# Kernel tuning notes

Hardware: AMD Instinct MI355X
Metric: run time of the kernel (lower is better)

Reference implementation:

```python
import jax, jax.numpy as jnp
import numpy as np

NUM_GROUPS = 32
EPS = 1e-6


def group_norm(x, gamma, beta):
    # x: [B, C, H, W]
    B, C, H, W = x.shape
    xg = x.reshape(B, NUM_GROUPS, C // NUM_GROUPS, H, W)
    mu = jnp.mean(xg, axis=(2, 3, 4), keepdims=True)
    var = jnp.var(xg, axis=(2, 3, 4), keepdims=True)
    xg = (xg - mu) * jax.lax.rsqrt(var + EPS)
    x = xg.reshape(B, C, H, W)
    return x * gamma[None, :, None, None] + beta[None, :, None, None]


def conv1x1(x, w, b):
    # x: [B, C, H, W], w: [O, C], b: [O]
    return jnp.einsum('bchw,oc->bohw', x, w) + b[None, :, None, None]


def setup_inputs() -> dict:
    key = jax.random.key(0)
    C = 512
    B, H, W = 4, 64, 64
    ks = jax.random.split(key, 10)
    s = 1.0 / np.sqrt(C)
    inp = {
        'x': jax.random.normal(ks[0], (B, C, H, W), dtype=jnp.float32),
        'gamma': jnp.ones((C,), dtype=jnp.float32),
        'beta': jnp.zeros((C,), dtype=jnp.float32),
        'wq': jax.random.normal(ks[1], (C, C), dtype=jnp.float32) * s,
        'bq': jnp.zeros((C,), dtype=jnp.float32),
        'wk': jax.random.normal(ks[2], (C, C), dtype=jnp.float32) * s,
        'bk': jnp.zeros((C,), dtype=jnp.float32),
        'wv': jax.random.normal(ks[3], (C, C), dtype=jnp.float32) * s,
        'bv': jnp.zeros((C,), dtype=jnp.float32),
        'wo': jax.random.normal(ks[4], (C, C), dtype=jnp.float32) * s,
        'bo': jnp.zeros((C,), dtype=jnp.float32),
    }
    return inp


def reference(x, gamma, beta, wq, bq, wk, bk, wv, bv, wo, bo):
    B, C, H, W = x.shape
    h = group_norm(x, gamma, beta)
    q = conv1x1(h, wq, bq).reshape(B, C, H * W)  # [B, C, S]
    k = conv1x1(h, wk, bk).reshape(B, C, H * W)
    v = conv1x1(h, wv, bv).reshape(B, C, H * W)
    scale = C ** (-0.5)
    # scores[b, S, s] = sum_c q[b, c, S] * k[b, c, s]
    w = jnp.einsum('bcS,bcs->bSs', q, k) * scale
    w = jax.nn.softmax(w, axis=-1)
    # out[b, c, S] = sum_s w[b, S, s] * v[b, c, s]
    hattn = jnp.einsum('bSs,bcs->bcS', w, v).reshape(B, C, H, W)
    out = conv1x1(hattn, wo, bo)
    return x + out
```

## Files before the change

kernel.cpp:

```cpp
#include <hip/hip_runtime.h>

#define B_   4
#define C_   512
#define S_   4096
#define G_   32
#define CPG_ 16
#define EPS_ 1e-6f

typedef unsigned short u16;
typedef __bf16 bf16x8 __attribute__((ext_vector_type(8)));
typedef float  f32x4  __attribute__((ext_vector_type(4)));

__device__ __forceinline__ u16 f2bf(float f) {
  unsigned u = __float_as_uint(f);
  u += 0x7fffu + ((u >> 16) & 1u);
  return (u16)(u >> 16);
}
__device__ __forceinline__ float bf2f(u16 h) {
  return __uint_as_float((unsigned)h << 16);
}

__device__ __forceinline__ void g2lds16(const void* g, void* l) {
  __builtin_amdgcn_global_load_lds(
      (const __attribute__((address_space(1))) void*)g,
      (__attribute__((address_space(3))) void*)l, 16, 0, 0);
}

#define BAR()    __builtin_amdgcn_s_barrier()
#define SCHED0() __builtin_amdgcn_sched_barrier(0)
#define WAITV4   asm volatile("s_waitcnt vmcnt(4)" ::: "memory")
#define WAITV3   asm volatile("s_waitcnt vmcnt(3)" ::: "memory")
#define WAITV0   asm volatile("s_waitcnt vmcnt(0)" ::: "memory")

__device__ __forceinline__ void xcd_swz(int& bx, int& by, int& bz) {
  const int gx = gridDim.x, gy = gridDim.y;
  const int nwg = gx * gy * (int)gridDim.z;
  const int flat = blockIdx.x + gx * (blockIdx.y + gy * blockIdx.z);
  const int q = nwg >> 3;
  const int nf = (flat & 7) * q + (flat >> 3);
  bx = nf % gx;
  const int r = nf / gx;
  by = r % gy;
  bz = r / gy;
}

__global__ __launch_bounds__(256) void f32_to_bf16(const float* __restrict__ in,
                                                   u16* __restrict__ out, int n) {
  int i = blockIdx.x * 256 + threadIdx.x;
  if (i < n) out[i] = f2bf(in[i]);
}

__global__ __launch_bounds__(256) void concat_bias(const float* __restrict__ a,
                                                   const float* __restrict__ b,
                                                   float* __restrict__ o) {
  int i = blockIdx.x * 256 + threadIdx.x;
  o[i] = (i < 512) ? a[i] : b[i - 512];
}

__global__ __launch_bounds__(256) void gn_stats(const float* __restrict__ x,
                                                float* __restrict__ stats) {
  const int bg = blockIdx.x;
  const float4* p4 = (const float4*)(x + (size_t)bg * (CPG_ * S_));
  float s = 0.f, ss = 0.f;
  const int tid = threadIdx.x;
  for (int i = tid; i < CPG_ * S_ / 4; i += 256) {
    float4 v = p4[i];
    s  += v.x + v.y + v.z + v.w;
    ss += v.x * v.x + v.y * v.y + v.z * v.z + v.w * v.w;
  }
#pragma unroll
  for (int o = 32; o; o >>= 1) { s += __shfl_xor(s, o, 64); ss += __shfl_xor(ss, o, 64); }
  __shared__ float sm[8];
  const int wid = tid >> 6, lane = tid & 63;
  if (lane == 0) { sm[wid * 2] = s; sm[wid * 2 + 1] = ss; }
  __syncthreads();
  if (tid == 0) {
    s  = sm[0] + sm[2] + sm[4] + sm[6];
    ss = sm[1] + sm[3] + sm[5] + sm[7];
    const float inv = 1.f / (float)(CPG_ * S_);
    float mu = s * inv;
    float var = ss * inv - mu * mu;
    stats[bg * 2]     = mu;
    stats[bg * 2 + 1] = rsqrtf(var + EPS_);
  }
}

__global__ __launch_bounds__(256) void gn_apply_t(const float* __restrict__ x,
                                                  const float* __restrict__ gamma,
                                                  const float* __restrict__ beta,
                                                  const float* __restrict__ stats,
                                                  u16* __restrict__ ht) {
  __shared__ float tile[32][33];
  const int b = blockIdx.z, c0 = blockIdx.y * 32, s0 = blockIdx.x * 32;
  const int tx = threadIdx.x, ty = threadIdx.y;
#pragma unroll
  for (int i = 0; i < 4; ++i) {
    const int c  = c0 + ty + i * 8;
    const float mu = stats[(b * G_ + (c >> 4)) * 2];
    const float rs = stats[(b * G_ + (c >> 4)) * 2 + 1];
    const float v  = x[((size_t)b * C_ + c) * S_ + s0 + tx];
    tile[ty + i * 8][tx] = (v - mu) * rs * gamma[c] + beta[c];
  }
  __syncthreads();
#pragma unroll
  for (int i = 0; i < 4; ++i) {
    const int s = s0 + ty + i * 8;
    ht[((size_t)b * S_ + s) * C_ + c0 + tx] = f2bf(tile[tx][ty + i * 8]);
  }
}

#define STAGE_A(T, KS) do {                                                  \
    const int _sl = (2 * (T) + (KS)) & 3;                                    \
    const size_t _ko = (size_t)(T) * 64 + (KS) * 32;                         \
    g2lds16(Asrc + _ko,  &As[_sl][wid * 512]);                               \
    g2lds16(Asrc2 + _ko, &As[_sl][4096 + wid * 512]);                        \
  } while (0)
#define STAGE_B(T, KS) do {                                                  \
    const int _sl = (2 * (T) + (KS)) & 3;                                    \
    const size_t _ko = (size_t)(T) * 64 + (KS) * 32;                         \
    g2lds16(Bsrc + _ko,  &Bs[_sl][wid * 512]);                               \
    g2lds16(Bsrc2 + _ko, &Bs[_sl][4096 + wid * 512]);                        \
  } while (0)
#define LDB4(SL)                                                             \
  _Pragma("unroll") for (int i = 0; i < 4; ++i)                              \
      bfr[i] = *(const bf16x8*)&Bs[(SL)][bbase + i * 512];
#define LDA4(SL, MH)                                                         \
  _Pragma("unroll") for (int i = 0; i < 4; ++i)                              \
      af[i] = *(const bf16x8*)&As[(SL)][abase + ((MH) * 4 + i) * 512];
#define MFMA16(MH) do {                                                      \
    __builtin_amdgcn_s_setprio(1);                                           \
    _Pragma("unroll") for (int mi = 0; mi < 4; ++mi)                         \
    _Pragma("unroll") for (int ni = 0; ni < 4; ++ni)                         \
      acc[(MH) * 4 + mi][ni] = __builtin_amdgcn_mfma_f32_16x16x32_bf16(      \
          af[mi], bfr[ni], acc[(MH) * 4 + mi][ni], 0, 0, 0);                 \
    __builtin_amdgcn_s_setprio(0);                                           \
  } while (0)

template <int BIAS_MODE>
__global__ __launch_bounds__(512, 2) void gemm256(
    const u16* __restrict__ Ag, int lda, long sA,
    const u16* __restrict__ Bg, int ldb, long sB,
    u16* __restrict__ Cg, int ldc, long sC,
    const float* __restrict__ bias, float alpha, int K) {
  __shared__ u16 As[4][8192];
  __shared__ u16 Bs[4][8192];
  int bx, by, bz;
  xcd_swz(bx, by, bz);
  const u16* A  = Ag + (size_t)bz * sA;
  const u16* Bm = Bg + (size_t)bz * sB;
  u16* Cb = Cg + (size_t)bz * sC;
  const int bm = by * 256, bn = bx * 256;
  const int tid = threadIdx.x;
  const int wid = tid >> 6, lane = tid & 63;
  const int wm = (wid >> 2) * 128, wn = (wid & 3) * 64;
  const int lr = lane & 15, lh = lane >> 4;

  const int srow = wid * 16 + (lane >> 2);
  const int sg   = (lane & 3) ^ ((srow >> 1) & 3);
  const u16* Asrc  = A  + (size_t)(bm + srow) * lda + sg * 8;
  const u16* Asrc2 = Asrc + (size_t)128 * lda;
  const u16* Bsrc  = Bm + (size_t)(bn + srow) * ldb + sg * 8;
  const u16* Bsrc2 = Bsrc + (size_t)128 * ldb;

  const int swz   = (lh ^ ((lr >> 1) & 3)) << 3;
  const int abase = (wm + lr) * 32 + swz;
  const int bbase = (wn + lr) * 32 + swz;

  float bias_v[4] = {0.f, 0.f, 0.f, 0.f};
  if (BIAS_MODE == 1) {
#pragma unroll
    for (int nf = 0; nf < 4; ++nf) bias_v[nf] = bias[bn + wn + nf * 16 + lr];
  }
  SCHED0();

  f32x4 acc[8][4];
  const f32x4 zero = {0.f, 0.f, 0.f, 0.f};
#pragma unroll
  for (int i = 0; i < 8; ++i)
#pragma unroll
    for (int j = 0; j < 4; ++j) acc[i][j] = zero;

  STAGE_A(0, 0); STAGE_B(0, 0); STAGE_A(0, 1); STAGE_B(0, 1);

  const int nt = K >> 6;
  for (int t = 0; t < nt; ++t) {
    const int s0 = (2 * t) & 3, s1 = s0 + 1;
    const bool pre = (t + 1 < nt);
    bf16x8 bfr[4], af[4];
    WAITV4;
    BAR(); SCHED0();
    LDB4(s0);
    LDA4(s0, 0);
    if (pre) STAGE_A(t + 1, 0);
    MFMA16(0);
    BAR(); SCHED0();
    LDA4(s0, 1);
    if (pre) STAGE_B(t + 1, 0);
    MFMA16(1);
    if (pre) { WAITV4; } else { WAITV0; }
    BAR(); SCHED0();
    LDB4(s1);
    LDA4(s1, 0);
    if (pre) STAGE_A(t + 1, 1);
    MFMA16(0);
    BAR(); SCHED0();
    LDA4(s1, 1);
    if (pre) STAGE_B(t + 1, 1);
    MFMA16(1);
  }
  SCHED0();

#pragma unroll
  for (int mf = 0; mf < 8; ++mf) {
    const int row0 = bm + wm + mf * 16 + lh * 4;
#pragma unroll
    for (int nf = 0; nf < 4; ++nf) {
      const int col = bn + wn + nf * 16 + lr;
#pragma unroll
      for (int r = 0; r < 4; ++r)
        Cb[(size_t)(row0 + r) * ldc + col] = f2bf(acc[mf][nf][r] * alpha + bias_v[nf]);
    }
  }
}

__global__ __launch_bounds__(512, 2) void gemm256pv(
    const u16* __restrict__ Ag, int lda, long sA,
    const u16* __restrict__ Bg, int ldb, long sB,
    u16* __restrict__ Cg, int ldc, long sC, int K) {
  __shared__ u16 As[4][8192];
  __shared__ u16 Bs[4][4096];
  int bx, by, bz;
  xcd_swz(bx, by, bz);
  const u16* A  = Ag + (size_t)bz * sA;
  const u16* Bm = Bg + (size_t)bz * sB;
  u16* Cb = Cg + (size_t)bz * sC;
  const int bm = by * 256, bn = bx * 128;
  const int tid = threadIdx.x;
  const int wid = tid >> 6, lane = tid & 63;
  const int wm = (wid >> 1) * 64, wn = (wid & 1) * 64;
  const int lr = lane & 15, lh = lane >> 4;

  const int srow = wid * 16 + (lane >> 2);
  const int sg   = (lane & 3) ^ ((srow >> 1) & 3);
  const u16* Asrc  = A  + (size_t)(bm + srow) * lda + sg * 8;
  const u16* Asrc2 = Asrc + (size_t)128 * lda;
  const u16* Bsrc  = Bm + (size_t)(bn + srow) * ldb + sg * 8;

  const int swz   = (lh ^ ((lr >> 1) & 3)) << 3;
  const int abase = (wm + lr) * 32 + swz;
  const int bbase = (wn + lr) * 32 + swz;

#define PSTAGE_A(T, KS) do {                                                 \
    const int _sl = (2 * (T) + (KS)) & 3;                                    \
    const size_t _ko = (size_t)(T) * 64 + (KS) * 32;                         \
    g2lds16(Asrc + _ko,  &As[_sl][wid * 512]);                               \
    g2lds16(Asrc2 + _ko, &As[_sl][4096 + wid * 512]);                        \
  } while (0)
#define PSTAGE_B(T, KS) do {                                                 \
    const int _sl = (2 * (T) + (KS)) & 3;                                    \
    const size_t _ko = (size_t)(T) * 64 + (KS) * 32;                         \
    g2lds16(Bsrc + _ko, &Bs[_sl][wid * 512]);                                \
  } while (0)

  f32x4 acc[4][4];
  const f32x4 zero = {0.f, 0.f, 0.f, 0.f};
#pragma unroll
  for (int i = 0; i < 4; ++i)
#pragma unroll
    for (int j = 0; j < 4; ++j) acc[i][j] = zero;

  PSTAGE_A(0, 0); PSTAGE_B(0, 0); PSTAGE_A(0, 1); PSTAGE_B(0, 1);

  const int nt = K >> 6;
  for (int t = 0; t < nt; ++t) {
    const int s0 = (2 * t) & 3, s1 = s0 + 1;
    const bool pre = (t + 1 < nt);
    bf16x8 bfr[4], af[4];
    WAITV3;
    BAR(); SCHED0();
    _Pragma("unroll") for (int i = 0; i < 4; ++i)
        bfr[i] = *(const bf16x8*)&Bs[s0][bbase + i * 512];
    _Pragma("unroll") for (int i = 0; i < 4; ++i)
        af[i] = *(const bf16x8*)&As[s0][abase + i * 512];
    if (pre) { PSTAGE_A(t + 1, 0); PSTAGE_B(t + 1, 0); }
    __builtin_amdgcn_s_setprio(1);
#pragma unroll
    for (int mi = 0; mi < 4; ++mi)
#pragma unroll
      for (int ni = 0; ni < 4; ++ni)
        acc[mi][ni] = __builtin_amdgcn_mfma_f32_16x16x32_bf16(af[mi], bfr[ni], acc[mi][ni], 0, 0, 0);
    __builtin_amdgcn_s_setprio(0);
    if (pre) { WAITV3; } else { WAITV0; }
    BAR(); SCHED0();
    _Pragma("unroll") for (int i = 0; i < 4; ++i)
        bfr[i] = *(const bf16x8*)&Bs[s1][bbase + i * 512];
    _Pragma("unroll") for (int i = 0; i < 4; ++i)
        af[i] = *(const bf16x8*)&As[s1][abase + i * 512];
    if (pre) { PSTAGE_A(t + 1, 1); PSTAGE_B(t + 1, 1); }
    __builtin_amdgcn_s_setprio(1);
#pragma unroll
    for (int mi = 0; mi < 4; ++mi)
#pragma unroll
      for (int ni = 0; ni < 4; ++ni)
        acc[mi][ni] = __builtin_amdgcn_mfma_f32_16x16x32_bf16(af[mi], bfr[ni], acc[mi][ni], 0, 0, 0);
    __builtin_amdgcn_s_setprio(0);
  }
  SCHED0();

#pragma unroll
  for (int mf = 0; mf < 4; ++mf) {
    const int row0 = bm + wm + mf * 16 + lh * 4;
#pragma unroll
    for (int nf = 0; nf < 4; ++nf) {
      const int col = bn + wn + nf * 16 + lr;
#pragma unroll
      for (int r = 0; r < 4; ++r)
        Cb[(size_t)(row0 + r) * ldc + col] = f2bf(acc[mf][nf][r]);
    }
  }
}

#define GBM 128
#define GBN 128
#define GBK 64

template <int BIAS_MODE, int OUT_MODE>
__global__ __launch_bounds__(256) void gemm_abT(
    const u16* __restrict__ Ag, int lda, long sA,
    const u16* __restrict__ Bg, int ldb, long sB,
    void* __restrict__ Cg, int ldc, long sC,
    const float* __restrict__ bias, float alpha,
    const float* __restrict__ xres, int K) {
  __shared__ u16 As[GBM * GBK];
  __shared__ u16 Bs[GBN * GBK];
  const int bz = blockIdx.z;
  const u16* A    = Ag + (size_t)bz * sA;
  const u16* Bmat = Bg + (size_t)bz * sB;
  const int bm = blockIdx.y * GBM, bn = blockIdx.x * GBN;
  const int tid = threadIdx.x;
  const int wid = tid >> 6, lane = tid & 63;
  const int wm = (wid >> 1) * 64, wn = (wid & 1) * 64;
  const int lr = lane & 15, lh = lane >> 4;
  const int srow = lane >> 3, scol = (lane & 7) * 8;

  f32x4 acc[4][4];
  const f32x4 zero = {0.f, 0.f, 0.f, 0.f};
#pragma unroll
  for (int i = 0; i < 4; ++i)
#pragma unroll
    for (int j = 0; j < 4; ++j) acc[i][j] = zero;

  for (int k0 = 0; k0 < K; k0 += GBK) {
    __syncthreads();
#pragma unroll
    for (int i = 0; i < 4; ++i) {
      const int chunk = wid * 4 + i;
      const int row   = chunk * 8 + srow;
      g2lds16(A    + (size_t)(bm + row) * lda + (k0 + scol), &As[chunk * 512]);
      g2lds16(Bmat + (size_t)(bn + row) * ldb + (k0 + scol), &Bs[chunk * 512]);
    }
    __syncthreads();
#pragma unroll
    for (int ks = 0; ks < 2; ++ks) {
      bf16x8 a_[4], b_[4];
#pragma unroll
      for (int m = 0; m < 4; ++m)
        a_[m] = *(const bf16x8*)&As[(wm + m * 16 + lr) * GBK + ks * 32 + lh * 8];
#pragma unroll
      for (int n = 0; n < 4; ++n)
        b_[n] = *(const bf16x8*)&Bs[(wn + n * 16 + lr) * GBK + ks * 32 + lh * 8];
#pragma unroll
      for (int m = 0; m < 4; ++m)
#pragma unroll
        for (int n = 0; n < 4; ++n)
          acc[m][n] = __builtin_amdgcn_mfma_f32_16x16x32_bf16(a_[m], b_[n], acc[m][n], 0, 0, 0);
    }
  }

  if (OUT_MODE == 0) {
    u16* Cb = (u16*)Cg + (size_t)bz * sC;
#pragma unroll
    for (int m = 0; m < 4; ++m) {
      const int row0 = bm + wm + m * 16 + lh * 4;
#pragma unroll
      for (int n = 0; n < 4; ++n) {
        const int col = bn + wn + n * 16 + lr;
        float bn_ = (BIAS_MODE == 1) ? bias[col] : 0.f;
#pragma unroll
        for (int r = 0; r < 4; ++r) {
          float bb = (BIAS_MODE == 2) ? bias[row0 + r] : bn_;
          Cb[(size_t)(row0 + r) * ldc + col] = f2bf(acc[m][n][r] * alpha + bb);
        }
      }
    }
  } else {
    float* Ob = (float*)Cg;
#pragma unroll
    for (int m = 0; m < 4; ++m) {
      const int row0 = bm + wm + m * 16 + lh * 4;
#pragma unroll
      for (int n = 0; n < 4; ++n) {
        const int col = bn + wn + n * 16 + lr;
        const int bb = col >> 12, sp = col & (S_ - 1);
#pragma unroll
        for (int r = 0; r < 4; ++r) {
          const int o = row0 + r;
          const size_t idx = ((size_t)bb * C_ + o) * S_ + sp;
          Ob[idx] = acc[m][n][r] * alpha + bias[o] + xres[idx];
        }
      }
    }
  }
}

__global__ __launch_bounds__(256) void softmax_rows(u16* __restrict__ sc) {
  const size_t base = ((size_t)blockIdx.y * S_ + blockIdx.x) * S_;
  uint4* r4 = (uint4*)(sc + base);
  const int tid = threadIdx.x;
  uint4 u0 = r4[tid], u1 = r4[tid + 256];
  float f[16];
  {
    const unsigned* pu = (const unsigned*)&u0;
    const unsigned* pv = (const unsigned*)&u1;
#pragma unroll
    for (int i = 0; i < 4; ++i) {
      f[2 * i]     = bf2f((u16)(pu[i] & 0xffffu));
      f[2 * i + 1] = bf2f((u16)(pu[i] >> 16));
      f[8 + 2 * i]     = bf2f((u16)(pv[i] & 0xffffu));
      f[8 + 2 * i + 1] = bf2f((u16)(pv[i] >> 16));
    }
  }
  float mx = f[0];
#pragma unroll
  for (int i = 1; i < 16; ++i) mx = fmaxf(mx, f[i]);
#pragma unroll
  for (int o = 32; o; o >>= 1) mx = fmaxf(mx, __shfl_xor(mx, o, 64));
  __shared__ float red[8];
  const int wid = tid >> 6, lane = tid & 63;
  if (lane == 0) red[wid] = mx;
  __syncthreads();
  mx = fmaxf(fmaxf(red[0], red[1]), fmaxf(red[2], red[3]));
  float s = 0.f;
#pragma unroll
  for (int i = 0; i < 16; ++i) { f[i] = __expf(f[i] - mx); s += f[i]; }
#pragma unroll
  for (int o = 32; o; o >>= 1) s += __shfl_xor(s, o, 64);
  if (lane == 0) red[4 + wid] = s;
  __syncthreads();
  s = red[4] + red[5] + red[6] + red[7];
  const float inv = 1.f / s;
  unsigned o0[4], o1[4];
#pragma unroll
  for (int i = 0; i < 4; ++i) {
    o0[i] = (unsigned)f2bf(f[2 * i] * inv)     | ((unsigned)f2bf(f[2 * i + 1] * inv) << 16);
    o1[i] = (unsigned)f2bf(f[8 + 2 * i] * inv) | ((unsigned)f2bf(f[8 + 2 * i + 1] * inv) << 16);
  }
  r4[tid]       = *(uint4*)o0;
  r4[tid + 256] = *(uint4*)o1;
}

extern "C" void kernel_launch(void* const* d_in, const int* in_sizes, int n_in,
                              void* d_out, int out_size, void* d_ws, size_t ws_size,
                              hipStream_t stream) {
  const float* x     = (const float*)d_in[0];
  const float* gamma = (const float*)d_in[1];
  const float* beta  = (const float*)d_in[2];
  const float* wq = (const float*)d_in[3];
  const float* bq = (const float*)d_in[4];
  const float* wk = (const float*)d_in[5];
  const float* bk = (const float*)d_in[6];
  const float* wv = (const float*)d_in[7];
  const float* bv = (const float*)d_in[8];
  const float* wo = (const float*)d_in[9];
  const float* bo = (const float*)d_in[10];
  float* out = (float*)d_out;

  char* ws = (char*)d_ws;
  float* stats = (float*)ws;
  u16* wqb = (u16*)(ws + 1024);
  u16* wkb = wqb + 262144;
  u16* wvb = wkb + 262144;
  u16* wob = wvb + 262144;
  float* bqk = (float*)(wob + 262144);
  u16* ht  = (u16*)((char*)bqk + 4096);
  u16* qkt = ht + 8388608;
  u16* vv  = qkt + 16777216;
  u16* sc  = vv + 8388608;
  u16* ha  = qkt;

  f32_to_bf16<<<1024, 256, 0, stream>>>(wq, wqb, 262144);
  f32_to_bf16<<<1024, 256, 0, stream>>>(wk, wkb, 262144);
  f32_to_bf16<<<1024, 256, 0, stream>>>(wv, wvb, 262144);
  f32_to_bf16<<<1024, 256, 0, stream>>>(wo, wob, 262144);
  concat_bias<<<4, 256, 0, stream>>>(bq, bk, bqk);

  gn_stats<<<128, 256, 0, stream>>>(x, stats);
  gn_apply_t<<<dim3(128, 16, 4), dim3(32, 8), 0, stream>>>(x, gamma, beta, stats, ht);

  gemm256<1><<<dim3(4, 64, 1), 512, 0, stream>>>(ht, 512, 0, wqb, 512, 0,
                                                 qkt, 1024, 0, bqk, 1.f, 512);
  gemm_abT<2, 0><<<dim3(128, 4, 1), 256, 0, stream>>>(wvb, 512, 0, ht, 512, 0,
                                                      vv, 16384, 0, bv, 1.f, nullptr, 512);
  gemm256<0><<<dim3(16, 16, 4), 512, 0, stream>>>(qkt, 1024, 4194304, qkt + 512, 1024, 4194304,
                                                  sc, 4096, 16777216, nullptr,
                                                  0.04419417382415922f, 512);
  softmax_rows<<<dim3(4096, 4), 256, 0, stream>>>(sc);
  gemm256pv<<<dim3(4, 16, 4), 512, 0, stream>>>(sc, 4096, 16777216, vv, 16384, 4096,
                                                ha, 512, 2097152, 4096);
  gemm_abT<2, 1><<<dim3(128, 4, 1), 256, 0, stream>>>(wob, 512, 0, ha, 512, 0,
                                                      out, 0, 0, bo, 1.f, x, 512);
}
```

Before: 323.7 us.

## Shrink GEMM LDS ring to double buffer and raise occupancy to four blocks

The 256-tile GEMM kernels drop from a 4-slot LDS ring to a 2-slot double buffer and prefetch one half-K-step ahead with full vmcnt(0) waits. This halves LDS use so launch bounds can request four blocks per CU. The PV kernel is generalised with bias/alpha and reused for the QK projection, giving a 256x128 tile and twice as many blocks. The trade-off is a shallower prefetch pipeline with stricter waits, plus register pressure from 8x4 accumulators at higher occupancy, which could spill or leave load latency exposed.

```diff
diff --git a/kernel.cpp b/kernel.cpp
--- a/kernel.cpp
+++ b/kernel.cpp
@@ -28,8 +28,6 @@
 
 #define BAR()    __builtin_amdgcn_s_barrier()
 #define SCHED0() __builtin_amdgcn_sched_barrier(0)
-#define WAITV4   asm volatile("s_waitcnt vmcnt(4)" ::: "memory")
-#define WAITV3   asm volatile("s_waitcnt vmcnt(3)" ::: "memory")
 #define WAITV0   asm volatile("s_waitcnt vmcnt(0)" ::: "memory")
 
 __device__ __forceinline__ void xcd_swz(int& bx, int& by, int& bz) {
@@ -109,18 +107,6 @@
   }
 }
 
-#define STAGE_A(T, KS) do {                                                  \
-    const int _sl = (2 * (T) + (KS)) & 3;                                    \
-    const size_t _ko = (size_t)(T) * 64 + (KS) * 32;                         \
-    g2lds16(Asrc + _ko,  &As[_sl][wid * 512]);                               \
-    g2lds16(Asrc2 + _ko, &As[_sl][4096 + wid * 512]);                        \
-  } while (0)
-#define STAGE_B(T, KS) do {                                                  \
-    const int _sl = (2 * (T) + (KS)) & 3;                                    \
-    const size_t _ko = (size_t)(T) * 64 + (KS) * 32;                         \
-    g2lds16(Bsrc + _ko,  &Bs[_sl][wid * 512]);                               \
-    g2lds16(Bsrc2 + _ko, &Bs[_sl][4096 + wid * 512]);                        \
-  } while (0)
 #define LDB4(SL)                                                             \
   _Pragma("unroll") for (int i = 0; i < 4; ++i)                              \
       bfr[i] = *(const bf16x8*)&Bs[(SL)][bbase + i * 512];
@@ -137,13 +123,13 @@
   } while (0)
 
 template <int BIAS_MODE>
-__global__ __launch_bounds__(512, 2) void gemm256(
+__global__ __launch_bounds__(512, 4) void gemm256(
     const u16* __restrict__ Ag, int lda, long sA,
     const u16* __restrict__ Bg, int ldb, long sB,
     u16* __restrict__ Cg, int ldc, long sC,
     const float* __restrict__ bias, float alpha, int K) {
-  __shared__ u16 As[4][8192];
-  __shared__ u16 Bs[4][8192];
+  __shared__ u16 As[2][8192];
+  __shared__ u16 Bs[2][8192];
   int bx, by, bz;
   xcd_swz(bx, by, bz);
   const u16* A  = Ag + (size_t)bz * sA;
@@ -171,7 +157,6 @@
 #pragma unroll
     for (int nf = 0; nf < 4; ++nf) bias_v[nf] = bias[bn + wn + nf * 16 + lr];
   }
-  SCHED0();
 
   f32x4 acc[8][4];
   const f32x4 zero = {0.f, 0.f, 0.f, 0.f};
@@ -180,34 +165,32 @@
 #pragma unroll
     for (int j = 0; j < 4; ++j) acc[i][j] = zero;
 
-  STAGE_A(0, 0); STAGE_B(0, 0); STAGE_A(0, 1); STAGE_B(0, 1);
-
+#define STAGE2(T, KS) do {                                                   \
+    const size_t _ko = (size_t)(T) * 64 + (KS) * 32;                         \
+    g2lds16(Asrc + _ko,  &As[(KS)][wid * 512]);                              \
+    g2lds16(Asrc2 + _ko, &As[(KS)][4096 + wid * 512]);                       \
+    g2lds16(Bsrc + _ko,  &Bs[(KS)][wid * 512]);                              \
+    g2lds16(Bsrc2 + _ko, &Bs[(KS)][4096 + wid * 512]);                       \
+  } while (0)
+
+  STAGE2(0, 0);
   const int nt = K >> 6;
   for (int t = 0; t < nt; ++t) {
-    const int s0 = (2 * t) & 3, s1 = s0 + 1;
-    const bool pre = (t + 1 < nt);
     bf16x8 bfr[4], af[4];
-    WAITV4;
+    WAITV0;
     BAR(); SCHED0();
-    LDB4(s0);
-    LDA4(s0, 0);
-    if (pre) STAGE_A(t + 1, 0);
-    MFMA16(0);
+    STAGE2(t, 1);
+    LDB4(0);
+    LDA4(0, 0); MFMA16(0);
+    LDA4(0, 1); MFMA16(1);
+    WAITV0;
     BAR(); SCHED0();
-    LDA4(s0, 1);
-    if (pre) STAGE_B(t + 1, 0);
-    MFMA16(1);
-    if (pre) { WAITV4; } else { WAITV0; }
-    BAR(); SCHED0();
-    LDB4(s1);
-    LDA4(s1, 0);
-    if (pre) STAGE_A(t + 1, 1);
-    MFMA16(0);
-    BAR(); SCHED0();
-    LDA4(s1, 1);
-    if (pre) STAGE_B(t + 1, 1);
-    MFMA16(1);
-  }
+    if (t + 1 < nt) STAGE2(t + 1, 0);
+    LDB4(1);
+    LDA4(1, 0); MFMA16(0);
+    LDA4(1, 1); MFMA16(1);
+  }
+#undef STAGE2
   SCHED0();
 
 #pragma unroll
@@ -223,12 +206,14 @@
   }
 }
 
-__global__ __launch_bounds__(512, 2) void gemm256pv(
+template <int BIAS_MODE>
+__global__ __launch_bounds__(512, 4) void gemm256n128(
     const u16* __restrict__ Ag, int lda, long sA,
     const u16* __restrict__ Bg, int ldb, long sB,
-    u16* __restrict__ Cg, int ldc, long sC, int K) {
-  __shared__ u16 As[4][8192];
-  __shared__ u16 Bs[4][4096];
+    u16* __restrict__ Cg, int ldc, long sC,
+    const float* __restrict__ bias, float alpha, int K) {
+  __shared__ u16 As[2][8192];
+  __shared__ u16 Bs[2][4096];
   int bx, by, bz;
   xcd_swz(bx, by, bz);
   const u16* A  = Ag + (size_t)bz * sA;
@@ -250,17 +235,11 @@
   const int abase = (wm + lr) * 32 + swz;
   const int bbase = (wn + lr) * 32 + swz;
 
-#define PSTAGE_A(T, KS) do {                                                 \
-    const int _sl = (2 * (T) + (KS)) & 3;                                    \
-    const size_t _ko = (size_t)(T) * 64 + (KS) * 32;                         \
-    g2lds16(Asrc + _ko,  &As[_sl][wid * 512]);                               \
-    g2lds16(Asrc2 + _ko, &As[_sl][4096 + wid * 512]);                        \
-  } while (0)
-#define PSTAGE_B(T, KS) do {                                                 \
-    const int _sl = (2 * (T) + (KS)) & 3;                                    \
-    const size_t _ko = (size_t)(T) * 64 + (KS) * 32;                         \
-    g2lds16(Bsrc + _ko, &Bs[_sl][wid * 512]);                                \
-  } while (0)
+  float bias_v[4] = {0.f, 0.f, 0.f, 0.f};
+  if (BIAS_MODE == 1) {
+#pragma unroll
+    for (int nf = 0; nf < 4; ++nf) bias_v[nf] = bias[bn + wn + nf * 16 + lr];
+  }
 
   f32x4 acc[4][4];
   const f32x4 zero = {0.f, 0.f, 0.f, 0.f};
@@ -269,42 +248,31 @@
 #pragma unroll
     for (int j = 0; j < 4; ++j) acc[i][j] = zero;
 
-  PSTAGE_A(0, 0); PSTAGE_B(0, 0); PSTAGE_A(0, 1); PSTAGE_B(0, 1);
-
+#define PSTG(T, KS) do {                                                     \
+    const size_t _ko = (size_t)(T) * 64 + (KS) * 32;                         \
+    g2lds16(Asrc + _ko,  &As[(KS)][wid * 512]);                              \
+    g2lds16(Asrc2 + _ko, &As[(KS)][4096 + wid * 512]);                       \
+    g2lds16(Bsrc + _ko,  &Bs[(KS)][wid * 512]);                              \
+  } while (0)
+
+  PSTG(0, 0);
   const int nt = K >> 6;
   for (int t = 0; t < nt; ++t) {
-    const int s0 = (2 * t) & 3, s1 = s0 + 1;
-    const bool pre = (t + 1 < nt);
     bf16x8 bfr[4], af[4];
-    WAITV3;
+    WAITV0;
     BAR(); SCHED0();
-    _Pragma("unroll") for (int i = 0; i < 4; ++i)
-        bfr[i] = *(const bf16x8*)&Bs[s0][bbase + i * 512];
-    _Pragma("unroll") for (int i = 0; i < 4; ++i)
-        af[i] = *(const bf16x8*)&As[s0][abase + i * 512];
-    if (pre) { PSTAGE_A(t + 1, 0); PSTAGE_B(t + 1, 0); }
-    __builtin_amdgcn_s_setprio(1);
-#pragma unroll
-    for (int mi = 0; mi < 4; ++mi)
-#pragma unroll
-      for (int ni = 0; ni < 4; ++ni)
-        acc[mi][ni] = __builtin_amdgcn_mfma_f32_16x16x32_bf16(af[mi], bfr[ni], acc[mi][ni], 0, 0, 0);
-    __builtin_amdgcn_s_setprio(0);
-    if (pre) { WAITV3; } else { WAITV0; }
+    PSTG(t, 1);
+    LDB4(0);
+    LDA4(0, 0);
+    MFMA16(0);
+    WAITV0;
     BAR(); SCHED0();
-    _Pragma("unroll") for (int i = 0; i < 4; ++i)
-        bfr[i] = *(const bf16x8*)&Bs[s1][bbase + i * 512];
-    _Pragma("unroll") for (int i = 0; i < 4; ++i)
-        af[i] = *(const bf16x8*)&As[s1][abase + i * 512];
-    if (pre) { PSTAGE_A(t + 1, 1); PSTAGE_B(t + 1, 1); }
-    __builtin_amdgcn_s_setprio(1);
-#pragma unroll
-    for (int mi = 0; mi < 4; ++mi)
-#pragma unroll
-      for (int ni = 0; ni < 4; ++ni)
-        acc[mi][ni] = __builtin_amdgcn_mfma_f32_16x16x32_bf16(af[mi], bfr[ni], acc[mi][ni], 0, 0, 0);
-    __builtin_amdgcn_s_setprio(0);
-  }
+    if (t + 1 < nt) PSTG(t + 1, 0);
+    LDB4(1);
+    LDA4(1, 0);
+    MFMA16(0);
+  }
+#undef PSTG
   SCHED0();
 
 #pragma unroll
@@ -315,7 +283,7 @@
       const int col = bn + wn + nf * 16 + lr;
 #pragma unroll
       for (int r = 0; r < 4; ++r)
-        Cb[(size_t)(row0 + r) * ldc + col] = f2bf(acc[mf][nf][r]);
+        Cb[(size_t)(row0 + r) * ldc + col] = f2bf(acc[mf][nf][r] * alpha + bias_v[nf]);
     }
   }
 }
@@ -497,16 +465,16 @@
   gn_stats<<<128, 256, 0, stream>>>(x, stats);
   gn_apply_t<<<dim3(128, 16, 4), dim3(32, 8), 0, stream>>>(x, gamma, beta, stats, ht);
 
-  gemm256<1><<<dim3(4, 64, 1), 512, 0, stream>>>(ht, 512, 0, wqb, 512, 0,
-                                                 qkt, 1024, 0, bqk, 1.f, 512);
+  gemm256n128<1><<<dim3(8, 64, 1), 512, 0, stream>>>(ht, 512, 0, wqb, 512, 0,
+                                                     qkt, 1024, 0, bqk, 1.f, 512);
   gemm_abT<2, 0><<<dim3(128, 4, 1), 256, 0, stream>>>(wvb, 512, 0, ht, 512, 0,
                                                       vv, 16384, 0, bv, 1.f, nullptr, 512);
   gemm256<0><<<dim3(16, 16, 4), 512, 0, stream>>>(qkt, 1024, 4194304, qkt + 512, 1024, 4194304,
                                                   sc, 4096, 16777216, nullptr,
                                                   0.04419417382415922f, 512);
   softmax_rows<<<dim3(4096, 4), 256, 0, stream>>>(sc);
-  gemm256pv<<<dim3(4, 16, 4), 512, 0, stream>>>(sc, 4096, 16777216, vv, 16384, 4096,
-                                                ha, 512, 2097152, 4096);
+  gemm256n128<0><<<dim3(4, 16, 4), 512, 0, stream>>>(sc, 4096, 16777216, vv, 16384, 4096,
+                                                     ha, 512, 2097152, nullptr, 1.f, 4096);
   gemm_abT<2, 1><<<dim3(128, 4, 1), 256, 0, stream>>>(wob, 512, 0, ha, 512, 0,
                                                       out, 0, 0, bo, 1.f, x, 512);
 }
```

New measurement: 858.2 us. 165% more time.
